# Optimization experiments

Hardware: AMD Instinct MI355X
Metric: run time of the kernel (lower is better)

Reference implementation:

```python
import jax, jax.numpy as jnp
import numpy as np

KH = KW = 3
STRIDE = 1
PAD = 1
DIL = 1


def _bilinear_sample(x, py, px):
    """Zero-padded bilinear sampling.
    x: [B, C, H, W]; py, px: [B, K2, Ho, Wo] float sample coords.
    returns [B, C, K2, Ho, Wo].
    """
    B, C, H, W = x.shape
    y0 = jnp.floor(py)
    x0 = jnp.floor(px)
    wy1 = py - y0
    wx1 = px - x0
    wy0 = 1.0 - wy1
    wx0 = 1.0 - wx1
    xf = x.reshape(B, C, H * W)

    def gather(iy, ix):
        valid = (iy >= 0) & (iy <= H - 1) & (ix >= 0) & (ix <= W - 1)
        iyc = jnp.clip(iy, 0, H - 1).astype(jnp.int32)
        ixc = jnp.clip(ix, 0, W - 1).astype(jnp.int32)
        idx = (iyc * W + ixc).reshape(B, 1, -1)  # [B,1,K2*Ho*Wo]
        v = jnp.take_along_axis(xf, idx, axis=2)
        v = v.reshape(B, C, *iy.shape[1:])
        return v * valid[:, None].astype(x.dtype)

    return (gather(y0, x0) * (wy0 * wx0)[:, None]
            + gather(y0, x0 + 1) * (wy0 * wx1)[:, None]
            + gather(y0 + 1, x0) * (wy1 * wx0)[:, None]
            + gather(y0 + 1, x0 + 1) * (wy1 * wx1)[:, None])


def setup_inputs() -> dict:
    key = jax.random.key(0)
    k1, k2, k3, k4 = jax.random.split(key, 4)
    B, C, H, W = 8, 64, 128, 128
    Cout = 64
    K2 = KH * KW
    x = jax.random.normal(k1, (B, C, H, W), dtype=jnp.float32)
    offset = jax.random.normal(k2, (B, 2 * K2, H, W), dtype=jnp.float32)
    mask = jax.random.uniform(k3, (B, K2, H, W), dtype=jnp.float32)
    n = C * KH * KW
    stdv = 1.0 / np.sqrt(n)
    weight = jax.random.uniform(k4, (Cout, C, KH, KW), dtype=jnp.float32,
                                minval=-stdv, maxval=stdv)
    bias = jnp.zeros((Cout,), dtype=jnp.float32)
    return {"x": x, "offset": offset, "mask": mask, "weight": weight, "bias": bias}


def reference(x, offset, mask, weight, bias):
    B, C, H, W = x.shape
    Cout, Cin, kh, kw = weight.shape
    K2 = kh * kw
    Ho = (H + 2 * PAD - (DIL * (kh - 1) + 1)) // STRIDE + 1
    Wo = (W + 2 * PAD - (DIL * (kw - 1) + 1)) // STRIDE + 1
    # offset channels come interleaved per kernel location: ::2 -> x, 1::2 -> y
    off = offset.reshape(B, K2, 2, Ho, Wo)
    dx = off[:, :, 0]  # [B,K2,Ho,Wo]
    dy = off[:, :, 1]
    base_y = (STRIDE * jnp.arange(Ho) - PAD).astype(x.dtype)  # [Ho]
    base_x = (STRIDE * jnp.arange(Wo) - PAD).astype(x.dtype)  # [Wo]
    ky = (DIL * jnp.arange(kh)).astype(x.dtype)
    kx = (DIL * jnp.arange(kw)).astype(x.dtype)
    koff_y = jnp.repeat(ky, kw)  # [K2]
    koff_x = jnp.tile(kx, kh)    # [K2]
    py = base_y[None, None, :, None] + koff_y[None, :, None, None] + dy
    px = base_x[None, None, None, :] + koff_x[None, :, None, None] + dx
    sampled = _bilinear_sample(x, py, px)          # [B,C,K2,Ho,Wo]
    sampled = sampled * mask[:, None]              # modulation
    w = weight.reshape(Cout, Cin * K2)
    cols = sampled.reshape(B, Cin * K2, Ho, Wo)
    out = jnp.einsum('bqhw,oq->bohw', cols, w) + bias[None, :, None, None]
    return out
```

## Files before the change

kernel.cpp:

```cpp
#include <hip/hip_runtime.h>
#include <hip/hip_bf16.h>
#include <hip/hip_fp16.h>


constexpr int B    = 8;
constexpr int C    = 64;
constexpr int H    = 128;
constexpr int W    = 128;
constexpr int COUT = 64;
constexpr int K2   = 9;
constexpr int HW   = H * W;
constexpr int TPX  = 64;

typedef __attribute__((ext_vector_type(8))) short   short8;
typedef __attribute__((ext_vector_type(8))) _Float16 f16x8;
typedef __attribute__((ext_vector_type(4))) float   f32x4;

constexpr int LDSS = 72;

#define LDS_BARRIER() asm volatile("s_waitcnt lgkmcnt(0)\n\ts_barrier" ::: "memory")

__global__ __launch_bounds__(256) void transpose_x_kernel(
    const float* __restrict__ x, short* __restrict__ xt) {
    __shared__ float tbuf[64][65];
    const int blk  = blockIdx.x;
    const int b    = blk >> 8;
    const int hwb  = (blk & 255) * 64;
    const int lane = threadIdx.x & 63;
    const int grp  = threadIdx.x >> 6;
    const float* xb = x + (size_t)b * C * HW;
#pragma unroll
    for (int r = 0; r < 16; ++r) {
        const int c = grp * 16 + r;
        tbuf[c][lane] = xb[c * HW + hwb + lane];
    }
    __syncthreads();
    short* xo = xt + (size_t)b * HW * C;
#pragma unroll
    for (int r = 0; r < 16; ++r) {
        const int hw_l = grp * 16 + r;
        union { __half h; short s; } u;
        u.h = __float2half(tbuf[lane][hw_l]);
        xo[(size_t)(hwb + hw_l) * C + lane] = u.s;
    }
}

__global__ __launch_bounds__(256) void pack_w_kernel(
    const float* __restrict__ w, short* __restrict__ wfrag) {
    int id = blockIdx.x * blockDim.x + threadIdx.x;
    if (id >= COUT * C * K2) return;
    const int j    = id & 7;
    const int lane = (id >> 3) & 63;
    const int mt   = (id >> 9) & 3;
    const int kk   = (id >> 11) & 1;
    const int k    = id >> 12;
    const int m    = mt * 16 + (lane & 15);
    const int q    = lane >> 4;
    const int c    = kk * 32 + q * 8 + j;
    union { __half h; short s; } u;
    u.h = __float2half(w[(m * C + c) * K2 + k]);
    wfrag[id] = u.s;
}

__global__ __launch_bounds__(512, 4) void mdcn_pc_kernel(
    const short* __restrict__ xt,
    const float* __restrict__ offset,
    const float* __restrict__ mask,
    const short* __restrict__ wfrag,
    const float* __restrict__ bias,
    float* __restrict__ out) {

    __shared__ short smem[2][TPX * LDSS];
    __shared__ int4  pidx[K2 * TPX];
    __shared__ uint4 pwts[K2 * TPX];

    const int wg   = blockIdx.x;
    const int b    = wg & 7;
    const int t    = wg >> 3;
    const int ho   = t >> 1;
    const int px0  = (t & 1) * TPX;

    const int tid  = threadIdx.x;
    const int wave = tid >> 6;

    for (int f = tid; f < K2 * TPX; f += 512) {
        const int k = f >> 6;
        const int i = f & 63;
        const int wo = px0 + i;
        const int ky = k / 3, kx = k % 3;
        const float dx = offset[(((size_t)b * 2 * K2 + 2 * k    ) * H + ho) * W + wo];
        const float dy = offset[(((size_t)b * 2 * K2 + 2 * k + 1) * H + ho) * W + wo];
        const float mm = mask  [(((size_t)b * K2     + k        ) * H + ho) * W + wo];
        const float py = (float)(ho - 1 + ky) + dy;
        const float px = (float)(wo - 1 + kx) + dx;
        const float y0f = floorf(py), x0f = floorf(px);
        const float wy1 = py - y0f,   wx1 = px - x0f;
        const float wy0 = 1.0f - wy1, wx0 = 1.0f - wx1;
        const int iy0 = (int)y0f, ix0 = (int)x0f;
        const int iy1 = iy0 + 1,  ix1 = ix0 + 1;
        const bool vy0 = (iy0 >= 0) & (iy0 < H);
        const bool vy1 = (iy1 >= 0) & (iy1 < H);
        const bool vx0 = (ix0 >= 0) & (ix0 < W);
        const bool vx1 = (ix1 >= 0) & (ix1 < W);
        const float w00 = (vy0 & vx0) ? wy0 * wx0 * mm : 0.0f;
        const float w01 = (vy0 & vx1) ? wy0 * wx1 * mm : 0.0f;
        const float w10 = (vy1 & vx0) ? wy1 * wx0 * mm : 0.0f;
        const float w11 = (vy1 & vx1) ? wy1 * wx1 * mm : 0.0f;
        union { __half2 h2; unsigned u; } c0, c1, c2, c3;
        c0.h2 = __floats2half2_rn(w00, w00);
        c1.h2 = __floats2half2_rn(w01, w01);
        c2.h2 = __floats2half2_rn(w10, w10);
        c3.h2 = __floats2half2_rn(w11, w11);
        uint4 wv;
        wv.x = c0.u; wv.y = c1.u; wv.z = c2.u; wv.w = c3.u;
        const int cy0 = min(max(iy0, 0), H - 1);
        const int cy1 = min(max(iy1, 0), H - 1);
        const int cx0 = min(max(ix0, 0), W - 1);
        const int cx1 = min(max(ix1, 0), W - 1);
        int4 bv;
        bv.x = (cy0 * W + cx0) * (C * 2);
        bv.y = (cy0 * W + cx1) * (C * 2);
        bv.z = (cy1 * W + cx0) * (C * 2);
        bv.w = (cy1 * W + cx1) * (C * 2);
        pidx[f] = bv;
        pwts[f] = wv;
    }
    __syncthreads();

    if (wave < 4) {
        const int spx = tid >> 2;
        const int cq  = (tid & 3) * 16;
        const char* xb =
            (const char*)(xt + (size_t)b * HW * C) + cq * 2;

        for (int k = 0; k < K2; ++k) {
            const int4  bi = pidx[k * 64 + spx];
            const uint4 wu = pwts[k * 64 + spx];
            union { unsigned u; __half2 h2; } w0{wu.x}, w1{wu.y}, w2{wu.z}, w3{wu.w};
            const short* s00 = (const short*)(xb + bi.x);
            const short* s01 = (const short*)(xb + bi.y);
            const short* s10 = (const short*)(xb + bi.z);
            const short* s11 = (const short*)(xb + bi.w);

            short* dst = &smem[k & 1][spx * LDSS + cq];
#pragma unroll
            for (int h = 0; h < 2; ++h) {
                union U8 { short8 s; __half2 h2[4]; };
                const U8 g00{*(const short8*)(s00 + h * 8)};
                const U8 g01{*(const short8*)(s01 + h * 8)};
                const U8 g10{*(const short8*)(s10 + h * 8)};
                const U8 g11{*(const short8*)(s11 + h * 8)};
                U8 rr;
#pragma unroll
                for (int p = 0; p < 4; ++p) {
                    rr.h2[p] = __hfma2(g11.h2[p], w3.h2,
                               __hfma2(g10.h2[p], w2.h2,
                               __hfma2(g01.h2[p], w1.h2,
                               __hmul2(g00.h2[p], w0.h2))));
                }
                *(short8*)(dst + h * 8) = rr.s;
            }
            LDS_BARRIER();
        }
    } else {
        const int widx = wave - 4;
        const int lane = tid & 63;
        const int col  = lane & 15;
        const int q    = lane >> 4;
        const int pix  = widx * 16 + col;
        const f16x8* wf = (const f16x8*)wfrag;

        f32x4 acc[4];
#pragma unroll
        for (int mt = 0; mt < 4; ++mt) acc[mt] = (f32x4)0.0f;

        for (int k = 0; k < K2; ++k) {
            LDS_BARRIER();
            f16x8 af[8];
#pragma unroll
            for (int i = 0; i < 8; ++i) af[i] = wf[(k * 8 + i) * 64 + lane];
#pragma unroll
            for (int kk = 0; kk < 2; ++kk) {
                const f16x8 bfrag =
                    *(const f16x8*)(&smem[k & 1][pix * LDSS + kk * 32 + q * 8]);
#pragma unroll
                for (int mt = 0; mt < 4; ++mt)
                    acc[mt] = __builtin_amdgcn_mfma_f32_16x16x32_f16(
                        af[kk * 4 + mt], bfrag, acc[mt], 0, 0, 0);
            }
        }

        const int wo = px0 + pix;
#pragma unroll
        for (int mt = 0; mt < 4; ++mt) {
#pragma unroll
            for (int r = 0; r < 4; ++r) {
                const int o = mt * 16 + q * 4 + r;
                out[(((size_t)b * COUT + o) * H + ho) * W + wo] =
                    acc[mt][r] + bias[o];
            }
        }
    }
}

__global__ __launch_bounds__(256) void mdcn_direct_kernel(
    const float* __restrict__ x, const float* __restrict__ offset,
    const float* __restrict__ mask, const float* __restrict__ wsrc,
    const float* __restrict__ bias, float* __restrict__ out) {
    const int p  = blockIdx.x * blockDim.x + threadIdx.x;
    const int wo = p & (W - 1);
    const int ho = (p >> 7) & (H - 1);
    const int b  = p >> 14;
    float acc[COUT];
#pragma unroll
    for (int o = 0; o < COUT; ++o) acc[o] = bias[o];
    const float* xb = x + b * C * HW;
    for (int k = 0; k < K2; ++k) {
        const int ky = k / 3, kx = k % 3;
        const float dx = offset[((b * 2 * K2 + 2 * k    ) * H + ho) * W + wo];
        const float dy = offset[((b * 2 * K2 + 2 * k + 1) * H + ho) * W + wo];
        const float m  = mask  [((b * K2     + k        ) * H + ho) * W + wo];
        const float py = (float)(ho - 1 + ky) + dy;
        const float px = (float)(wo - 1 + kx) + dx;
        const float y0f = floorf(py), x0f = floorf(px);
        const float wy1 = py - y0f, wx1 = px - x0f;
        const float wy0 = 1.0f - wy1, wx0 = 1.0f - wx1;
        const int iy0 = (int)y0f, ix0 = (int)x0f;
        const int iy1 = iy0 + 1, ix1 = ix0 + 1;
        const bool vy0 = (iy0 >= 0) & (iy0 < H);
        const bool vy1 = (iy1 >= 0) & (iy1 < H);
        const bool vx0 = (ix0 >= 0) & (ix0 < W);
        const bool vx1 = (ix1 >= 0) & (ix1 < W);
        const float w00 = (vy0 & vx0) ? wy0 * wx0 * m : 0.0f;
        const float w01 = (vy0 & vx1) ? wy0 * wx1 * m : 0.0f;
        const float w10 = (vy1 & vx0) ? wy1 * wx0 * m : 0.0f;
        const float w11 = (vy1 & vx1) ? wy1 * wx1 * m : 0.0f;
        const int cy0 = min(max(iy0, 0), H - 1);
        const int cy1 = min(max(iy1, 0), H - 1);
        const int cx0 = min(max(ix0, 0), W - 1);
        const int cx1 = min(max(ix1, 0), W - 1);
        const int o00 = cy0 * W + cx0, o01 = cy0 * W + cx1;
        const int o10 = cy1 * W + cx0, o11 = cy1 * W + cx1;
        for (int c = 0; c < C; ++c) {
            const float* xp = xb + c * HW;
            const float val = w00 * xp[o00] + w01 * xp[o01] +
                              w10 * xp[o10] + w11 * xp[o11];
#pragma unroll
            for (int o = 0; o < COUT; ++o)
                acc[o] += wsrc[(o * C + c) * K2 + k] * val;
        }
    }
    float* op = out + ((size_t)b * COUT) * HW + ho * W + wo;
#pragma unroll
    for (int o = 0; o < COUT; ++o) op[o * HW] = acc[o];
}

extern "C" void kernel_launch(void* const* d_in, const int* in_sizes, int n_in,
                              void* d_out, int out_size, void* d_ws, size_t ws_size,
                              hipStream_t stream) {
    const float* x      = (const float*)d_in[0];
    const float* offset = (const float*)d_in[1];
    const float* mask   = (const float*)d_in[2];
    const float* weight = (const float*)d_in[3];
    const float* bias   = (const float*)d_in[4];
    float* out          = (float*)d_out;

    const size_t xt_bytes = (size_t)B * HW * C * sizeof(short);
    const size_t wf_bytes = (size_t)COUT * C * K2 * sizeof(short);
    if (ws_size >= xt_bytes + wf_bytes) {
        short* xt    = (short*)d_ws;
        short* wfrag = (short*)((char*)d_ws + xt_bytes);
        transpose_x_kernel<<<B * (HW / 64), 256, 0, stream>>>(x, xt);
        pack_w_kernel<<<(COUT * C * K2 + 255) / 256, 256, 0, stream>>>(weight, wfrag);
        mdcn_pc_kernel<<<2 * B * H, 512, 0, stream>>>(xt, offset, mask, wfrag, bias, out);
    } else {
        mdcn_direct_kernel<<<(B * HW) / 256, 256, 0, stream>>>(
            x, offset, mask, weight, bias, out);
    }
}
```

Measured before the change: 138.7 us.

## Split MFMA tile across waves by output channel and prefetch weight fragments

The consumer waves previously each owned 16 pixels and loaded all 64 output-channel weight fragments per kernel tap. Now each wave owns 16 output channels across all 64 pixels, so it loads only 2 weight fragments per tap and reads 4 B fragments from LDS instead of one. Weight fragments for the next tap are double-buffered in registers and loaded before the current tap's MFMAs to hide global latency. This lowers global weight traffic and register pressure at the cost of more LDS reads, and the output store pattern changes to per-channel rows with contiguous pixels.

```diff
diff --git a/kernel.cpp b/kernel.cpp
--- a/kernel.cpp
+++ b/kernel.cpp
@@ -12,9 +12,9 @@
 constexpr int HW   = H * W;
 constexpr int TPX  = 64;
 
-typedef __attribute__((ext_vector_type(8))) short   short8;
+typedef __attribute__((ext_vector_type(8))) short    short8;
 typedef __attribute__((ext_vector_type(8))) _Float16 f16x8;
-typedef __attribute__((ext_vector_type(4))) float   f32x4;
+typedef __attribute__((ext_vector_type(4))) float    f32x4;
 
 constexpr int LDSS = 72;
 
@@ -163,41 +163,51 @@
             LDS_BARRIER();
         }
     } else {
-        const int widx = wave - 4;
+        const int w    = wave - 4;
         const int lane = tid & 63;
         const int col  = lane & 15;
         const int q    = lane >> 4;
-        const int pix  = widx * 16 + col;
         const f16x8* wf = (const f16x8*)wfrag;
 
         f32x4 acc[4];
 #pragma unroll
-        for (int mt = 0; mt < 4; ++mt) acc[mt] = (f32x4)0.0f;
-
+        for (int nt = 0; nt < 4; ++nt) acc[nt] = (f32x4)0.0f;
+
+        f16x8 afa[2], afb[2];
+#pragma unroll
+        for (int kk = 0; kk < 2; ++kk)
+            afa[kk] = wf[(kk * 4 + w) * 64 + lane];
+
+#pragma unroll
         for (int k = 0; k < K2; ++k) {
+            auto& af  = (k & 1) ? afb : afa;
+            auto& afn = (k & 1) ? afa : afb;
             LDS_BARRIER();
-            f16x8 af[8];
-#pragma unroll
-            for (int i = 0; i < 8; ++i) af[i] = wf[(k * 8 + i) * 64 + lane];
+            if (k + 1 < K2) {
+#pragma unroll
+                for (int kk = 0; kk < 2; ++kk)
+                    afn[kk] = wf[((k + 1) * 8 + kk * 4 + w) * 64 + lane];
+            }
 #pragma unroll
             for (int kk = 0; kk < 2; ++kk) {
-                const f16x8 bfrag =
-                    *(const f16x8*)(&smem[k & 1][pix * LDSS + kk * 32 + q * 8]);
-#pragma unroll
-                for (int mt = 0; mt < 4; ++mt)
-                    acc[mt] = __builtin_amdgcn_mfma_f32_16x16x32_f16(
-                        af[kk * 4 + mt], bfrag, acc[mt], 0, 0, 0);
-            }
-        }
-
-        const int wo = px0 + pix;
-#pragma unroll
-        for (int mt = 0; mt < 4; ++mt) {
+#pragma unroll
+                for (int nt = 0; nt < 4; ++nt) {
+                    const f16x8 bfrag = *(const f16x8*)(
+                        &smem[k & 1][(nt * 16 + col) * LDSS + kk * 32 + q * 8]);
+                    acc[nt] = __builtin_amdgcn_mfma_f32_16x16x32_f16(
+                        af[kk], bfrag, acc[nt], 0, 0, 0);
+                }
+            }
+        }
+
+#pragma unroll
+        for (int nt = 0; nt < 4; ++nt) {
+            const int wo = px0 + nt * 16 + col;
 #pragma unroll
             for (int r = 0; r < 4; ++r) {
-                const int o = mt * 16 + q * 4 + r;
+                const int o = w * 16 + q * 4 + r;
                 out[(((size_t)b * COUT + o) * H + ho) * W + wo] =
-                    acc[mt][r] + bias[o];
+                    acc[nt][r] + bias[o];
             }
         }
     }
```

Measured after the change: 129.8 us. -6.4%, faster.
